# Performance work log

Measured on AMD Instinct MI355X. Metric: run time of the kernel, lower is better.

## Reference

```python
import jax, jax.numpy as jnp
import numpy as np

NUM_HEADS = 16
HEAD_DIM = 64
COMP_RATIO = 8


def setup_inputs() -> dict:
    key = jax.random.key(0)
    ks = jax.random.split(key, 6)
    d_model = NUM_HEADS * HEAD_DIM  # 1024
    B, S = 2, 8192
    scale = 1.0 / np.sqrt(d_model)
    x = jax.random.normal(ks[0], (B, S, d_model), dtype=jnp.float32)
    Wq = jax.random.normal(ks[1], (d_model, NUM_HEADS * HEAD_DIM), dtype=jnp.float32) * scale
    Wk = jax.random.normal(ks[2], (d_model, NUM_HEADS * HEAD_DIM), dtype=jnp.float32) * scale
    Wv = jax.random.normal(ks[3], (d_model, NUM_HEADS * HEAD_DIM), dtype=jnp.float32) * scale
    Wo = jax.random.normal(ks[4], (NUM_HEADS * HEAD_DIM, d_model), dtype=jnp.float32) * scale
    bq = jnp.zeros((NUM_HEADS * HEAD_DIM,), jnp.float32)
    bk = jnp.zeros((NUM_HEADS * HEAD_DIM,), jnp.float32)
    bv = jnp.zeros((NUM_HEADS * HEAD_DIM,), jnp.float32)
    bo = jnp.zeros((d_model,), jnp.float32)
    return {"x": x, "local_window_start": 4096, "Wq": Wq, "bq": bq,
            "Wk": Wk, "bk": bk, "Wv": Wv, "bv": bv, "Wo": Wo, "bo": bo}


def reference(x, local_window_start, Wq, bq, Wk, bk, Wv, bv, Wo, bo):
    B, S, D = x.shape
    H, Hd, R = NUM_HEADS, HEAD_DIM, COMP_RATIO
    if local_window_start <= R:
        return jnp.zeros_like(x)
    num_pools = local_window_start // R
    if num_pools == 0:
        return jnp.zeros_like(x)
    trunc = num_pools * R
    # avg-pool compression of tokens before the local window
    compressed = x[:, :trunc, :].reshape(B, num_pools, R, D).mean(axis=2)  # (B, P, D)
    # projections
    q = (x @ Wq + bq).reshape(B, S, H, Hd).transpose(0, 2, 1, 3)            # (B,H,S,Hd)
    k = (compressed @ Wk + bk).reshape(B, num_pools, H, Hd).transpose(0, 2, 1, 3)  # (B,H,P,Hd)
    v = (compressed @ Wv + bv).reshape(B, num_pools, H, Hd).transpose(0, 2, 1, 3)
    scale = 1.0 / jnp.sqrt(jnp.float32(Hd))
    scores = jnp.einsum('bhqd,bhkd->bhqk', q, k) * scale                    # (B,H,S,P)
    # causal mask: a query can attend to a pool only if the pool fully precedes it
    q_pos = jnp.arange(S)[:, None]
    pool_end = (jnp.arange(num_pools) + 1) * R
    mask = q_pos >= pool_end[None, :]                                       # (S, P)
    scores = jnp.where(mask[None, None], scores, -1e9)
    attn = jax.nn.softmax(scores, axis=-1)
    out = jnp.einsum('bhqk,bhkd->bhqd', attn, v)                            # (B,H,S,Hd)
    out = out.transpose(0, 2, 1, 3).reshape(B, S, H * Hd)
    return out @ Wo + bo
```

## Files before the change

kernel.cpp:

```cpp
#include <hip/hip_runtime.h>
#include <hip/hip_bf16.h>


typedef __attribute__((ext_vector_type(8))) short bf16x8;
typedef __attribute__((ext_vector_type(4))) short bf16x4;
typedef __attribute__((ext_vector_type(4))) float f32x4;

#define MFMA_BF16(a, b, c) __builtin_amdgcn_mfma_f32_16x16x32_bf16((a), (b), (c), 0, 0, 0)

__device__ __forceinline__ unsigned short f2bu(float x) {
  __hip_bfloat16 b = __float2bfloat16(x);
  return __builtin_bit_cast(unsigned short, b);
}

__device__ __forceinline__ unsigned cvtpk(float lo, float hi) {
  unsigned r;
  asm("v_cvt_pk_bf16_f32 %0, %1, %2" : "=v"(r) : "v"(lo), "v"(hi));
  return r;
}

__device__ __forceinline__ float fexp2(float x) {
  float r;
  asm("v_exp_f32 %0, %1" : "=v"(r) : "v"(x));
  return r;
}

__device__ __forceinline__ void gload_lds16(const void* g, void* l) {
  __builtin_amdgcn_global_load_lds(
      (const __attribute__((address_space(1))) unsigned*)(g),
      (__attribute__((address_space(3))) unsigned*)(l), 16, 0, 0);
}

__device__ __forceinline__ unsigned ldsaddr(const void* p) {
  return (unsigned)(unsigned long long)(const __attribute__((address_space(3))) char*)p;
}

__global__ void cast_compress_kernel(const float* __restrict__ x,
                                     __hip_bfloat16* __restrict__ xb,
                                     __hip_bfloat16* __restrict__ cb) {
  const int blk = blockIdx.x;
  const int b = blk >> 10, g = blk & 1023;
  const int d = threadIdx.x * 4;
  const size_t rb = ((size_t)(b * 8192 + g * 8)) * 1024 + d;
  float4 a = {0.f, 0.f, 0.f, 0.f};
#pragma unroll
  for (int r = 0; r < 8; ++r) {
    const float4 v = *(const float4*)&x[rb + (size_t)r * 1024];
    ushort4 o;
    o.x = f2bu(v.x); o.y = f2bu(v.y); o.z = f2bu(v.z); o.w = f2bu(v.w);
    *(ushort4*)&xb[rb + (size_t)r * 1024] = o;
    a.x += v.x; a.y += v.y; a.z += v.z; a.w += v.w;
  }
  if (g < 512) {
    ushort4 o;
    o.x = f2bu(a.x * 0.125f); o.y = f2bu(a.y * 0.125f);
    o.z = f2bu(a.z * 0.125f); o.w = f2bu(a.w * 0.125f);
    *(ushort4*)&cb[((size_t)(b * 512 + g)) * 1024 + d] = o;
  }
}

__global__ void transpose_w_kernel(const float* __restrict__ w0, const float* __restrict__ w1,
                                   const float* __restrict__ w2, const float* __restrict__ w3,
                                   __hip_bfloat16* __restrict__ t0, __hip_bfloat16* __restrict__ t1,
                                   __hip_bfloat16* __restrict__ t2, __hip_bfloat16* __restrict__ t3) {
  const float* W; __hip_bfloat16* T;
  switch (blockIdx.z) {
    case 0: W = w0; T = t0; break;
    case 1: W = w1; T = t1; break;
    case 2: W = w2; T = t2; break;
    default: W = w3; T = t3; break;
  }
  __shared__ float tile[32][33];
  const int tx = threadIdx.x, ty = threadIdx.y;
  const int k0 = blockIdx.x * 32, n0 = blockIdx.y * 32;
#pragma unroll
  for (int j = 0; j < 4; ++j) {
    const int kk = ty + j * 8;
    tile[kk][tx] = W[(size_t)(k0 + kk) * 1024 + n0 + tx];
  }
  __syncthreads();
#pragma unroll
  for (int j = 0; j < 4; ++j) {
    const int nn = ty + j * 8;
    T[(size_t)(n0 + nn) * 1024 + k0 + tx] = __float2bfloat16(tile[tx][nn]);
  }
}


#define STAGE(SPTR, SROWBASE, STILE, SLDSOFF)                                  \
  {                                                                            \
    const int _t = (STILE) < NT ? (STILE) : 0;                                 \
    const size_t _kb = (size_t)_t * 128;                                       \
    gload_lds16((const char*)(SPTR) + ((size_t)((SROWBASE) + srow0) * K) * 2 + _kb + scb0, \
                ldsC + (SLDSOFF) + wave * 1024);                               \
    gload_lds16((const char*)(SPTR) + ((size_t)((SROWBASE) + srow0 + 64) * K) * 2 + _kb + scb0, \
                ldsC + (SLDSOFF) + 8192 + wave * 1024);                        \
  }

#define MM4(MR, AF0, AF1)                                                      \
  acc[MR][0] = MFMA_BF16(AF0, bf00, acc[MR][0]);                               \
  acc[MR][1] = MFMA_BF16(AF0, bf10, acc[MR][1]);                               \
  acc[MR][2] = MFMA_BF16(AF0, bf20, acc[MR][2]);                               \
  acc[MR][3] = MFMA_BF16(AF0, bf30, acc[MR][3]);                               \
  acc[MR][0] = MFMA_BF16(AF1, bf01, acc[MR][0]);                               \
  acc[MR][1] = MFMA_BF16(AF1, bf11, acc[MR][1]);                               \
  acc[MR][2] = MFMA_BF16(AF1, bf21, acc[MR][2]);                               \
  acc[MR][3] = MFMA_BF16(AF1, bf31, acc[MR][3]);

#define PHASE(QM, DB, LOADB, SPTR, SROWBASE, STILE, SLDSOFF, DOVM)             \
  {                                                                            \
    bf16x8 af0, af1, af2, af3;                                                 \
    const unsigned ab = Ab0 + (DB)*32768u + (QM)*4096u;                        \
    asm volatile("ds_read_b128 %0, %1" : "=v"(af0) : "v"(ab));                 \
    asm volatile("ds_read_b128 %0, %1" : "=v"(af1) : "v"(ab ^ 64u));           \
    asm volatile("ds_read_b128 %0, %1" : "=v"(af2) : "v"(ab + 2048u));         \
    asm volatile("ds_read_b128 %0, %1" : "=v"(af3) : "v"((ab + 2048u) ^ 64u)); \
    if (LOADB) {                                                               \
      const unsigned bb = Bb0 + (DB)*32768u;                                   \
      asm volatile("ds_read_b128 %0, %1" : "=v"(bf00) : "v"(bb));              \
      asm volatile("ds_read_b128 %0, %1" : "=v"(bf01) : "v"(bb ^ 64u));        \
      asm volatile("ds_read_b128 %0, %1" : "=v"(bf10) : "v"(bb + 2048u));      \
      asm volatile("ds_read_b128 %0, %1" : "=v"(bf11) : "v"((bb + 2048u) ^ 64u)); \
      asm volatile("ds_read_b128 %0, %1" : "=v"(bf20) : "v"(bb + 4096u));      \
      asm volatile("ds_read_b128 %0, %1" : "=v"(bf21) : "v"((bb + 4096u) ^ 64u)); \
      asm volatile("ds_read_b128 %0, %1" : "=v"(bf30) : "v"(bb + 6144u));      \
      asm volatile("ds_read_b128 %0, %1" : "=v"(bf31) : "v"((bb + 6144u) ^ 64u)); \
    }                                                                          \
    STAGE(SPTR, SROWBASE, STILE, SLDSOFF)                                      \
    asm volatile("s_barrier" ::: "memory");                                    \
    asm volatile("s_waitcnt lgkmcnt(0)" ::: "memory");                         \
    __builtin_amdgcn_sched_barrier(0);                                         \
    __builtin_amdgcn_s_setprio(1);                                             \
    MM4((QM)*2 + 0, af0, af1)                                                  \
    MM4((QM)*2 + 1, af2, af3)                                                  \
    __builtin_amdgcn_s_setprio(0);                                             \
    if (DOVM) asm volatile("s_waitcnt vmcnt(4)" ::: "memory");                 \
    asm volatile("s_barrier" ::: "memory");                                    \
  }

template <typename OUT_T>
__global__ __launch_bounds__(512, 2) void gemm256_kernel(
    const __hip_bfloat16* __restrict__ A, const __hip_bfloat16* __restrict__ Bt,
    const float* __restrict__ bias, OUT_T* __restrict__ C, int M, int N, int K) {
  __shared__ alignas(16) char lds[131072];
  char* ldsC = lds;
  const int tid = threadIdx.x;
  const int wave = tid >> 6, lane = tid & 63;
  const int l15 = lane & 15, lg = lane >> 4;
  const int wm = wave >> 2, wn = wave & 3;

  const int nwg = gridDim.x, cpx = nwg >> 3;
  const int bid = blockIdx.x;
  const int swz = (bid & 7) * cpx + (bid >> 3);
  const int ncol = N >> 8;
  const int bn = swz % ncol, bm = swz / ncol;
  const long brow = (long)bm * 256;
  const long bcol = (long)bn * 256;

  const int NT = K >> 6;
  const int NITER = K >> 7;

  const int o0 = wave * 1024 + lane * 16;
  const int srow0 = o0 >> 7;
  const int scb0 = (o0 & 127) ^ ((srow0 & 7) << 4);

  const unsigned LB = ldsaddr(lds);
  const int off0 = (lg * 16) ^ ((l15 & 7) << 4);
  const unsigned Ab0 = LB + wm * 16384u + l15 * 128u + off0;
  const unsigned Bb0 = LB + 65536u + (wn >> 1) * 16384u + (wn & 1) * 8192u + l15 * 128u + off0;

  f32x4 acc[8][4];
#pragma unroll
  for (int m = 0; m < 8; ++m)
#pragma unroll
    for (int n = 0; n < 4; ++n) acc[m][n] = (f32x4){0.f, 0.f, 0.f, 0.f};

  bf16x8 bf00, bf01, bf10, bf11, bf20, bf21, bf30, bf31;

  STAGE(Bt, bcol + 128, 0, 81920)
  STAGE(Bt, bcol,       0, 65536)
  STAGE(A,  brow,       0, 0)
  STAGE(A,  brow + 128, 0, 16384)
  STAGE(Bt, bcol + 128, 1, 114688)
  STAGE(Bt, bcol,       1, 98304)
  asm volatile("s_waitcnt vmcnt(4)" ::: "memory");
  asm volatile("s_barrier" ::: "memory");

  for (int i = 0; i < NITER; ++i) {
    const int t0 = 2 * i;
    PHASE(0, 0, true,  A,  brow,       t0 + 1, 32768,  false)
    PHASE(1, 0, false, A,  brow + 128, t0 + 1, 49152,  false)
    PHASE(2, 0, false, Bt, bcol + 128, t0 + 2, 81920,  false)
    PHASE(3, 0, false, Bt, bcol,       t0 + 2, 65536,  true)
    PHASE(0, 1, true,  A,  brow,       t0 + 2, 0,      false)
    PHASE(1, 1, false, A,  brow + 128, t0 + 2, 16384,  false)
    PHASE(2, 1, false, Bt, bcol + 128, t0 + 3, 114688, false)
    PHASE(3, 1, false, Bt, bcol,       t0 + 3, 98304,  true)
  }

#pragma unroll
  for (int nn = 0; nn < 4; ++nn) {
    const long col = bcol + wn * 64 + nn * 16 + l15;
    const float bv = bias[col];
#pragma unroll
    for (int mr = 0; mr < 8; ++mr) {
      const long row = brow + wm * 128 + mr * 16 + lg * 4;
#pragma unroll
      for (int j = 0; j < 4; ++j) {
        const float v = acc[mr][nn][j] + bv;
        if constexpr (sizeof(OUT_T) == 2)
          C[(row + j) * N + col] = __float2bfloat16(v);
        else
          C[(row + j) * N + col] = v;
      }
    }
  }
}

__global__ __launch_bounds__(256, 2) void gemm_bt_dual_kernel(
    const __hip_bfloat16* __restrict__ A,
    const __hip_bfloat16* __restrict__ Bt0, const float* __restrict__ b0,
    __hip_bfloat16* __restrict__ C0,
    const __hip_bfloat16* __restrict__ Bt1, const float* __restrict__ b1,
    __hip_bfloat16* __restrict__ Vt, int M, int N, int K) {
  const int sel = blockIdx.x >= (unsigned)(N >> 7);
  const __hip_bfloat16* Bt = sel ? Bt1 : Bt0;
  const float* bias = sel ? b1 : b0;
  const int bx = blockIdx.x - sel * (N >> 7);

  __shared__ alignas(16) __hip_bfloat16 As[128 * 32];
  __shared__ alignas(16) __hip_bfloat16 Bs[128 * 32];
  const int tid = threadIdx.x;
  const int wave = tid >> 6, lane = tid & 63;
  const int l15 = lane & 15, lg = lane >> 4;
  const long brow = (long)blockIdx.y * 128;
  const long bcol = (long)bx * 128;
  const int wr = (wave >> 1) * 64;
  const int wc = (wave & 1) * 64;

  f32x4 acc[4][4];
#pragma unroll
  for (int m = 0; m < 4; ++m)
#pragma unroll
    for (int n = 0; n < 4; ++n) acc[m][n] = (f32x4){0.f, 0.f, 0.f, 0.f};

  for (int kt = 0; kt < K; kt += 32) {
#pragma unroll
    for (int j = 0; j < 2; ++j) {
      const int seg = wave * 2 + j;
      const int o = seg * 1024;
      const int ob = o + lane * 16;
      const int row = ob >> 6;
      const int cb = ob & 63;
      gload_lds16((const char*)A + ((brow + row) * (long)K + kt) * 2 + cb, (char*)As + o);
      gload_lds16((const char*)Bt + ((bcol + row) * (long)K + kt) * 2 + cb, (char*)Bs + o);
    }
    __syncthreads();
    bf16x8 af[4], bfr[4];
#pragma unroll
    for (int m = 0; m < 4; ++m)
      af[m] = *(const bf16x8*)&As[(wr + m * 16 + l15) * 32 + lg * 8];
#pragma unroll
    for (int n = 0; n < 4; ++n)
      bfr[n] = *(const bf16x8*)&Bs[(wc + n * 16 + l15) * 32 + lg * 8];
#pragma unroll
    for (int m = 0; m < 4; ++m)
#pragma unroll
      for (int n = 0; n < 4; ++n)
        acc[m][n] = MFMA_BF16(af[m], bfr[n], acc[m][n]);
    __syncthreads();
  }

#pragma unroll
  for (int m = 0; m < 4; ++m)
#pragma unroll
    for (int n = 0; n < 4; ++n) {
      const long col = bcol + wc + n * 16 + l15;
      const float bv = bias[col];
      const long row0 = brow + wr + m * 16 + lg * 4;
      if (!sel) {
#pragma unroll
        for (int r = 0; r < 4; ++r)
          C0[(row0 + r) * N + col] = __float2bfloat16(acc[m][n][r] + bv);
      } else {
        const int bb = (int)(row0 >> 9);
        const int p = (int)(row0 & 511);
        ushort4 w;
        w.x = f2bu(acc[m][n][0] + bv);
        w.y = f2bu(acc[m][n][1] + bv);
        w.z = f2bu(acc[m][n][2] + bv);
        w.w = f2bu(acc[m][n][3] + bv);
        *(ushort4*)&Vt[((size_t)(bb * 1024 + col)) * 512 + p] = w;
      }
    }
}

__global__ __launch_bounds__(512, 2) void attn_kernel(
    const __hip_bfloat16* __restrict__ Q,
    const __hip_bfloat16* __restrict__ Km,
    const __hip_bfloat16* __restrict__ Vt,
    __hip_bfloat16* __restrict__ O) {
  __shared__ alignas(16) __hip_bfloat16 Ks[512 * 64];
  __shared__ alignas(16) __hip_bfloat16 VT[64 * 512];
  const int bh = blockIdx.x;
  const int b = bh >> 4, h = bh & 15;
  const int tid = threadIdx.x, wave = tid >> 6, lane = tid & 63;
  const int l15 = lane & 15, lg = lane >> 4;
  const char* Kbase = (const char*)(Km + (size_t)b * 512 * 1024 + h * 64);
  const char* VtP = (const char*)(Vt + (size_t)bh * 32768);
  char* KsB = (char*)Ks;
  char* VTB = (char*)VT;

#pragma unroll
  for (int j = 0; j < 8; ++j) {
    const int seg = wave * 8 + j;
    const int p = seg * 8 + (lane >> 3);
    const int cb = ((lane & 7) * 16) ^ ((p & 7) << 4);
    gload_lds16(Kbase + (size_t)p * 2048 + cb, KsB + seg * 1024);
  }
#pragma unroll
  for (int j = 0; j < 8; ++j) {
    const int d = wave * 8 + j;
    const int cb = (lane * 16) ^ ((d & 7) << 4);
    gload_lds16(VtP + (size_t)d * 1024 + cb, VTB + d * 1024);
  }
  __syncthreads();

  constexpr float SC = 0.18033688011112042f;
  for (int itq = 0; itq < 4; ++itq) {
    const int q0 = (blockIdx.y + itq * 8) * 256 + wave * 32;
    const __hip_bfloat16* Qr0 = Q + ((size_t)(b * 8192 + q0 + l15)) * 1024 + h * 64;
    const __hip_bfloat16* Qr1 = Qr0 + (size_t)16 * 1024;
    const bf16x8 qa0 = *(const bf16x8*)(Qr0 + lg * 8);
    const bf16x8 qa1 = *(const bf16x8*)(Qr0 + 32 + lg * 8);
    const bf16x8 qb0 = *(const bf16x8*)(Qr1 + lg * 8);
    const bf16x8 qb1 = *(const bf16x8*)(Qr1 + 32 + lg * 8);

    float l0 = 0.f, l1 = 0.f;
    f32x4 o4[2][4];
#pragma unroll
    for (int g = 0; g < 2; ++g)
#pragma unroll
      for (int d = 0; d < 4; ++d) o4[g][d] = (f32x4){0.f, 0.f, 0.f, 0.f};

#pragma unroll
    for (int ch = 0; ch < 4; ++ch) {
      if (!(ch == 0 || q0 == 0 || q0 >= ch * 1024)) continue;

      f32x4 s[2][8];
#pragma unroll
      for (int cc = 0; cc < 8; ++cc) {
        const int p = ch * 128 + cc * 16 + l15;
        const int rb = p * 128;
        const int sw = (p & 7) << 4;
        const bf16x8 kf0 = *(const bf16x8*)(KsB + rb + ((lg * 16) ^ sw));
        const bf16x8 kf1 = *(const bf16x8*)(KsB + rb + ((lg * 16 + 64) ^ sw));
        f32x4 z0 = {0.f, 0.f, 0.f, 0.f};
        z0 = MFMA_BF16(kf0, qa0, z0);
        z0 = MFMA_BF16(kf1, qa1, z0);
        s[0][cc] = z0;
        f32x4 z1 = {0.f, 0.f, 0.f, 0.f};
        z1 = MFMA_BF16(kf0, qb0, z1);
        z1 = MFMA_BF16(kf1, qb1, z1);
        s[1][cc] = z1;
      }
      if (q0 < (ch + 1) * 1024) {
#pragma unroll
        for (int g = 0; g < 2; ++g) {
          const int qa = q0 + g * 16 + l15;
          const float mval = (qa >= 8) ? -1.0e9f : 0.f;
#pragma unroll
          for (int cc = 0; cc < 8; ++cc) {
            const int pb8 = (ch * 128 + cc * 16 + lg * 4 + 1) * 8;
#pragma unroll
            for (int r = 0; r < 4; ++r)
              if (qa < pb8 + r * 8) s[g][cc][r] = mval;
          }
        }
      }
#pragma unroll
      for (int cc = 0; cc < 8; ++cc)
#pragma unroll
        for (int r = 0; r < 4; ++r) {
          const float e0 = fexp2(s[0][cc][r] * SC);
          const float e1 = fexp2(s[1][cc][r] * SC);
          s[0][cc][r] = e0; l0 += e0;
          s[1][cc][r] = e1; l1 += e1;
        }
#pragma unroll
      for (int kc = 0; kc < 4; ++kc) {
        uint4 u0, u1;
        u0.x = cvtpk(s[0][kc * 2][0], s[0][kc * 2][1]);
        u0.y = cvtpk(s[0][kc * 2][2], s[0][kc * 2][3]);
        u0.z = cvtpk(s[0][kc * 2 + 1][0], s[0][kc * 2 + 1][1]);
        u0.w = cvtpk(s[0][kc * 2 + 1][2], s[0][kc * 2 + 1][3]);
        u1.x = cvtpk(s[1][kc * 2][0], s[1][kc * 2][1]);
        u1.y = cvtpk(s[1][kc * 2][2], s[1][kc * 2][3]);
        u1.z = cvtpk(s[1][kc * 2 + 1][0], s[1][kc * 2 + 1][1]);
        u1.w = cvtpk(s[1][kc * 2 + 1][2], s[1][kc * 2 + 1][3]);
        const bf16x8 p0 = __builtin_bit_cast(bf16x8, u0);
        const bf16x8 p1 = __builtin_bit_cast(bf16x8, u1);
        const int pbase = ch * 128 + kc * 32;
#pragma unroll
        for (int db = 0; db < 4; ++db) {
          const int d = db * 16 + l15;
          const int rowb = d * 1024;
          const int sw = (d & 7) << 4;
          const bf16x4 v0 = *(const bf16x4*)(VTB + rowb + (((pbase + lg * 4) * 2) ^ sw));
          const bf16x4 v1 = *(const bf16x4*)(VTB + rowb + (((pbase + 16 + lg * 4) * 2) ^ sw));
          const bf16x8 af = {v0[0], v0[1], v0[2], v0[3], v1[0], v1[1], v1[2], v1[3]};
          o4[0][db] = MFMA_BF16(af, p0, o4[0][db]);
          o4[1][db] = MFMA_BF16(af, p1, o4[1][db]);
        }
      }
    }
#pragma unroll
    for (int g = 0; g < 2; ++g) {
      float t = g ? l1 : l0;
      t += __shfl_xor(t, 16);
      t += __shfl_xor(t, 32);
      const float inv = 1.f / t;
      __hip_bfloat16* Op =
          O + ((size_t)(b * 8192 + q0 + g * 16 + l15)) * 1024 + h * 64 + lg * 4;
#pragma unroll
      for (int db = 0; db < 4; ++db) {
        uint2 w;
        w.x = cvtpk(o4[g][db][0] * inv, o4[g][db][1] * inv);
        w.y = cvtpk(o4[g][db][2] * inv, o4[g][db][3] * inv);
        *(uint2*)(Op + db * 16) = w;
      }
    }
  }
}

extern "C" void kernel_launch(void* const* d_in, const int* in_sizes, int n_in,
                              void* d_out, int out_size, void* d_ws, size_t ws_size,
                              hipStream_t stream) {
  const float* x  = (const float*)d_in[0];
  const float* Wq = (const float*)d_in[2];
  const float* bq = (const float*)d_in[3];
  const float* Wk = (const float*)d_in[4];
  const float* bk = (const float*)d_in[5];
  const float* Wv = (const float*)d_in[6];
  const float* bv = (const float*)d_in[7];
  const float* Wo = (const float*)d_in[8];
  const float* bo = (const float*)d_in[9];
  float* out = (float*)d_out;

  constexpr size_t SZ_XB = (size_t)16384 * 1024 * 2;
  constexpr size_t SZ_WT = (size_t)1024 * 1024 * 2;
  constexpr size_t SZ_CB = (size_t)1024 * 1024 * 2;
  char* ws = (char*)d_ws;
  __hip_bfloat16* xb   = (__hip_bfloat16*)ws;
  __hip_bfloat16* WqT  = (__hip_bfloat16*)(ws + SZ_XB);
  __hip_bfloat16* WkT  = (__hip_bfloat16*)(ws + SZ_XB + SZ_WT);
  __hip_bfloat16* WvT  = (__hip_bfloat16*)(ws + SZ_XB + 2 * SZ_WT);
  __hip_bfloat16* WoT  = (__hip_bfloat16*)(ws + SZ_XB + 3 * SZ_WT);
  __hip_bfloat16* cbuf = (__hip_bfloat16*)(ws + SZ_XB + 4 * SZ_WT);
  __hip_bfloat16* Qb   = (__hip_bfloat16*)(ws + SZ_XB + 4 * SZ_WT + SZ_CB);
  __hip_bfloat16* Kb   = (__hip_bfloat16*)(ws + SZ_XB + 4 * SZ_WT + SZ_CB + SZ_XB);
  __hip_bfloat16* Vtb  = (__hip_bfloat16*)(ws + SZ_XB + 4 * SZ_WT + SZ_CB + SZ_XB + SZ_CB);

  cast_compress_kernel<<<dim3(2048), dim3(256), 0, stream>>>(x, xb, cbuf);
  transpose_w_kernel<<<dim3(32, 32, 4), dim3(32, 8), 0, stream>>>(
      Wq, Wk, Wv, Wo, WqT, WkT, WvT, WoT);
  gemm256_kernel<__hip_bfloat16><<<dim3(256), dim3(512), 0, stream>>>(
      xb, WqT, bq, Qb, 16384, 1024, 1024);
  gemm_bt_dual_kernel<<<dim3(16, 8), dim3(256), 0, stream>>>(
      cbuf, WkT, bk, Kb, WvT, bv, Vtb, 1024, 1024, 1024);
  attn_kernel<<<dim3(32, 8), dim3(512), 0, stream>>>(Qb, Kb, Vtb, xb);
  gemm256_kernel<float><<<dim3(256), dim3(512), 0, stream>>>(
      xb, WoT, bo, out, 16384, 1024, 1024);
}
```

Before: 170.5 us.

## Merge prep kernels, balance attention query-tile order, add MFMA priority hints

```diff
diff --git a/kernel.cpp b/kernel.cpp
--- a/kernel.cpp
+++ b/kernel.cpp
@@ -35,54 +35,58 @@
   return (unsigned)(unsigned long long)(const __attribute__((address_space(3))) char*)p;
 }
 
-__global__ void cast_compress_kernel(const float* __restrict__ x,
-                                     __hip_bfloat16* __restrict__ xb,
-                                     __hip_bfloat16* __restrict__ cb) {
-  const int blk = blockIdx.x;
-  const int b = blk >> 10, g = blk & 1023;
-  const int d = threadIdx.x * 4;
-  const size_t rb = ((size_t)(b * 8192 + g * 8)) * 1024 + d;
-  float4 a = {0.f, 0.f, 0.f, 0.f};
-#pragma unroll
-  for (int r = 0; r < 8; ++r) {
-    const float4 v = *(const float4*)&x[rb + (size_t)r * 1024];
-    ushort4 o;
-    o.x = f2bu(v.x); o.y = f2bu(v.y); o.z = f2bu(v.z); o.w = f2bu(v.w);
-    *(ushort4*)&xb[rb + (size_t)r * 1024] = o;
-    a.x += v.x; a.y += v.y; a.z += v.z; a.w += v.w;
-  }
-  if (g < 512) {
-    ushort4 o;
-    o.x = f2bu(a.x * 0.125f); o.y = f2bu(a.y * 0.125f);
-    o.z = f2bu(a.z * 0.125f); o.w = f2bu(a.w * 0.125f);
-    *(ushort4*)&cb[((size_t)(b * 512 + g)) * 1024 + d] = o;
-  }
-}
-
-__global__ void transpose_w_kernel(const float* __restrict__ w0, const float* __restrict__ w1,
-                                   const float* __restrict__ w2, const float* __restrict__ w3,
-                                   __hip_bfloat16* __restrict__ t0, __hip_bfloat16* __restrict__ t1,
-                                   __hip_bfloat16* __restrict__ t2, __hip_bfloat16* __restrict__ t3) {
-  const float* W; __hip_bfloat16* T;
-  switch (blockIdx.z) {
-    case 0: W = w0; T = t0; break;
-    case 1: W = w1; T = t1; break;
-    case 2: W = w2; T = t2; break;
-    default: W = w3; T = t3; break;
-  }
+__global__ void prep_kernel(const float* __restrict__ x,
+                            __hip_bfloat16* __restrict__ xb,
+                            __hip_bfloat16* __restrict__ cb,
+                            const float* __restrict__ w0, const float* __restrict__ w1,
+                            const float* __restrict__ w2, const float* __restrict__ w3,
+                            __hip_bfloat16* __restrict__ t0, __hip_bfloat16* __restrict__ t1,
+                            __hip_bfloat16* __restrict__ t2, __hip_bfloat16* __restrict__ t3) {
   __shared__ float tile[32][33];
-  const int tx = threadIdx.x, ty = threadIdx.y;
-  const int k0 = blockIdx.x * 32, n0 = blockIdx.y * 32;
-#pragma unroll
-  for (int j = 0; j < 4; ++j) {
-    const int kk = ty + j * 8;
-    tile[kk][tx] = W[(size_t)(k0 + kk) * 1024 + n0 + tx];
-  }
-  __syncthreads();
-#pragma unroll
-  for (int j = 0; j < 4; ++j) {
-    const int nn = ty + j * 8;
-    T[(size_t)(n0 + nn) * 1024 + k0 + tx] = __float2bfloat16(tile[tx][nn]);
+  const int bid = blockIdx.x;
+  const int tid = threadIdx.x;
+  if (bid < 2048) {
+    const int b = bid >> 10, g = bid & 1023;
+    const int d = tid * 4;
+    const size_t rb = ((size_t)(b * 8192 + g * 8)) * 1024 + d;
+    float4 a = {0.f, 0.f, 0.f, 0.f};
+#pragma unroll
+    for (int r = 0; r < 8; ++r) {
+      const float4 v = *(const float4*)&x[rb + (size_t)r * 1024];
+      ushort4 o;
+      o.x = f2bu(v.x); o.y = f2bu(v.y); o.z = f2bu(v.z); o.w = f2bu(v.w);
+      *(ushort4*)&xb[rb + (size_t)r * 1024] = o;
+      a.x += v.x; a.y += v.y; a.z += v.z; a.w += v.w;
+    }
+    if (g < 512) {
+      ushort4 o;
+      o.x = f2bu(a.x * 0.125f); o.y = f2bu(a.y * 0.125f);
+      o.z = f2bu(a.z * 0.125f); o.w = f2bu(a.w * 0.125f);
+      *(ushort4*)&cb[((size_t)(b * 512 + g)) * 1024 + d] = o;
+    }
+  } else {
+    const int t = bid - 2048;
+    const int z = t >> 10, rem = t & 1023;
+    const int k0 = (rem & 31) * 32, n0 = (rem >> 5) * 32;
+    const float* W; __hip_bfloat16* T;
+    switch (z) {
+      case 0: W = w0; T = t0; break;
+      case 1: W = w1; T = t1; break;
+      case 2: W = w2; T = t2; break;
+      default: W = w3; T = t3; break;
+    }
+    const int tx = tid & 31, ty = tid >> 5;
+#pragma unroll
+    for (int j = 0; j < 4; ++j) {
+      const int kk = ty + j * 8;
+      tile[kk][tx] = W[(size_t)(k0 + kk) * 1024 + n0 + tx];
+    }
+    __syncthreads();
+#pragma unroll
+    for (int j = 0; j < 4; ++j) {
+      const int nn = ty + j * 8;
+      T[(size_t)(n0 + nn) * 1024 + k0 + tx] = __float2bfloat16(tile[tx][nn]);
+    }
   }
 }
 
@@ -328,7 +332,10 @@
 
   constexpr float SC = 0.18033688011112042f;
   for (int itq = 0; itq < 4; ++itq) {
-    const int q0 = (blockIdx.y + itq * 8) * 256 + wave * 32;
+    const int y = blockIdx.y;
+    const int sidx = (itq == 0) ? y : (itq == 1) ? 15 - y
+                   : (itq == 2) ? 16 + y : 31 - y;
+    const int q0 = sidx * 256 + wave * 32;
     const __hip_bfloat16* Qr0 = Q + ((size_t)(b * 8192 + q0 + l15)) * 1024 + h * 64;
     const __hip_bfloat16* Qr1 = Qr0 + (size_t)16 * 1024;
     const bf16x8 qa0 = *(const bf16x8*)(Qr0 + lg * 8);
@@ -348,6 +355,7 @@
       if (!(ch == 0 || q0 == 0 || q0 >= ch * 1024)) continue;
 
       f32x4 s[2][8];
+      __builtin_amdgcn_s_setprio(1);
 #pragma unroll
       for (int cc = 0; cc < 8; ++cc) {
         const int p = ch * 128 + cc * 16 + l15;
@@ -364,6 +372,7 @@
         z1 = MFMA_BF16(kf1, qb1, z1);
         s[1][cc] = z1;
       }
+      __builtin_amdgcn_s_setprio(0);
       if (q0 < (ch + 1) * 1024) {
 #pragma unroll
         for (int g = 0; g < 2; ++g) {
@@ -401,6 +410,7 @@
         const bf16x8 p0 = __builtin_bit_cast(bf16x8, u0);
         const bf16x8 p1 = __builtin_bit_cast(bf16x8, u1);
         const int pbase = ch * 128 + kc * 32;
+        __builtin_amdgcn_s_setprio(1);
 #pragma unroll
         for (int db = 0; db < 4; ++db) {
           const int d = db * 16 + l15;
@@ -412,6 +422,7 @@
           o4[0][db] = MFMA_BF16(af, p0, o4[0][db]);
           o4[1][db] = MFMA_BF16(af, p1, o4[1][db]);
         }
+        __builtin_amdgcn_s_setprio(0);
       }
     }
 #pragma unroll
@@ -461,9 +472,8 @@
   __hip_bfloat16* Kb   = (__hip_bfloat16*)(ws + SZ_XB + 4 * SZ_WT + SZ_CB + SZ_XB);
   __hip_bfloat16* Vtb  = (__hip_bfloat16*)(ws + SZ_XB + 4 * SZ_WT + SZ_CB + SZ_XB + SZ_CB);
 
-  cast_compress_kernel<<<dim3(2048), dim3(256), 0, stream>>>(x, xb, cbuf);
-  transpose_w_kernel<<<dim3(32, 32, 4), dim3(32, 8), 0, stream>>>(
-      Wq, Wk, Wv, Wo, WqT, WkT, WvT, WoT);
+  prep_kernel<<<dim3(6144), dim3(256), 0, stream>>>(
+      x, xb, cbuf, Wq, Wk, Wv, Wo, WqT, WkT, WvT, WoT);
   gemm256_kernel<__hip_bfloat16><<<dim3(256), dim3(512), 0, stream>>>(
       xb, WqT, bq, Qb, 16384, 1024, 1024);
   gemm_bt_dual_kernel<<<dim3(16, 8), dim3(256), 0, stream>>>(
```

After: 170.8 us. No clear change (+0.2%).
